# Kernel tuning notes

Hardware: AMD Instinct MI355X
Metric: run time of the kernel (lower is better)

## Reference

```python
import jax, jax.numpy as jnp
import numpy as np
from jax import lax

B, D, H, W = 1, 16, 128, 128
CIN, NPTS = 16, 100000
NEG = np.float32(-1e30)  # stands in for -inf at unoccupied voxels in max pooling


def _conv(x, wk):
    # Minkowski stride-1 conv at occupied sites == dense zero-padded conv masked to occupancy
    return lax.conv_general_dilated(x, wk, (1, 1, 1), 'SAME',
                                    dimension_numbers=('NCDHW', 'OIDHW', 'NCDHW'))


def _crelu(x, wk, occ):
    return jnp.where(occ, jax.nn.relu(_conv(x, wk)), 0.0)


def _mpool(x, occ, spatial):
    # Minkowski max pool: max over occupied voxels in the kernel window; output coords are
    # the stride-floored input coords (z halved). spatial=True -> kernel (3,3,3) else (3,1,1).
    xm = jnp.where(occ, x, NEG)
    win = (1, 1, 3, 3, 3) if spatial else (1, 1, 3, 1, 1)
    pad = [(0, 0), (0, 0), (1, 1), (1, 1), (1, 1)] if spatial else [(0, 0), (0, 0), (1, 1), (0, 0), (0, 0)]
    y = lax.reduce_window(xm, NEG, lax.max, win, (1, 1, 2, 1, 1), pad)
    occ2 = occ[:, :, 0::2] | occ[:, :, 1::2]
    return jnp.where(occ2, y, 0.0), occ2


def _forward(voxel_features, coors, ws, batch_size):
    b, d, h, w = coors[:, 0], coors[:, 1], coors[:, 2], coors[:, 3]
    cin = voxel_features.shape[1]
    grid = jnp.zeros((batch_size, D, H, W, cin), voxel_features.dtype).at[b, d, h, w].set(voxel_features)
    x = jnp.transpose(grid, (0, 4, 1, 2, 3))  # (B, C, D, H, W)
    occ = jnp.zeros((batch_size, 1, D, H, W), bool).at[b, 0, d, h, w].set(True)

    x = _crelu(x, ws[0], occ)
    x = _crelu(x, ws[1], occ)
    x, occ = _mpool(x, occ, True)
    for wk in ws[2:5]:
        x = _crelu(x, wk, occ)
    x, occ = _mpool(x, occ, True)
    for wk in ws[5:8]:
        x = _crelu(x, wk, occ)
    x, occ = _mpool(x, occ, False)  # kernel (3,1,1)
    n, c, dd, hh, ww = x.shape  # (B, 64, 2, H, W)
    return x.reshape(n, c * dd, hh, ww)


def setup_inputs():
    key = jax.random.key(0)
    ks = jax.random.split(key, 9)
    rng = np.random.default_rng(0)
    lin = rng.permutation(D * H * W)[:NPTS].astype(np.int64)  # unique occupied voxels
    d = (lin // (H * W)).astype(np.int32)
    h = ((lin // W) % H).astype(np.int32)
    w = (lin % W).astype(np.int32)
    coors = jnp.asarray(np.stack([np.zeros(NPTS, np.int32), d, h, w], axis=1))
    vf = jax.random.normal(ks[0], (NPTS, CIN), jnp.float32)

    def cw(k, o, i):
        return jax.random.normal(k, (o, i, 3, 3, 3), jnp.float32) * np.float32(1.0 / np.sqrt(i * 27))

    chans = [(32, CIN), (64, 32)] + [(64, 64)] * 6
    ws = {f"w{j + 1}": cw(ks[j + 1], o, i) for j, (o, i) in enumerate(chans)}
    return dict(voxel_features=vf, coors=coors, batch_size=B, **ws)


def reference(voxel_features, coors, batch_size, w1, w2, w3, w4, w5, w6, w7, w8):
    return _forward(voxel_features, coors, (w1, w2, w3, w4, w5, w6, w7, w8), batch_size)
```

## Files before the change

### kernel.cpp

```cpp
#include <hip/hip_runtime.h>
#include <stdint.h>

#define DEV __device__ __forceinline__

typedef float f32x4 __attribute__((ext_vector_type(4)));
typedef short s16x8 __attribute__((ext_vector_type(8)));
typedef unsigned int u32x4 __attribute__((ext_vector_type(4)));
typedef unsigned int u32x2 __attribute__((ext_vector_type(2)));

static constexpr int HM = 128, WM = 128;
static constexpr int HP = 130, WP = 130;

DEV unsigned short f2bf(float f) {
  unsigned int u = __float_as_uint(f);
  return (unsigned short)((u + 0x7fffu + ((u >> 16) & 1u)) >> 16);
}
DEV float bf2f(unsigned short s) { return __uint_as_float(((unsigned int)s) << 16); }

DEV void gll16(const void* g, void* l) {
  __builtin_amdgcn_global_load_lds((const unsigned int*)g, (unsigned int*)l, 16, 0, 0);
}

__global__ __launch_bounds__(256)
void scatter_k(const float* __restrict__ vf, const int* __restrict__ co,
               unsigned short* __restrict__ x,
               unsigned char* __restrict__ o0, unsigned char* __restrict__ o1,
               unsigned char* __restrict__ o2, unsigned char* __restrict__ o3,
               int npts) {
  int i = blockIdx.x * 256 + threadIdx.x;
  if (i >= npts) return;
  int d = co[i * 4 + 1], h = co[i * 4 + 2], w = co[i * 4 + 3];
  unsigned short* dst = x + (size_t)(((d + 1) * HP + (h + 1)) * WP + (w + 1)) * 32;
#pragma unroll
  for (int c = 0; c < 16; ++c) dst[c] = f2bf(vf[i * 16 + c]);
  int hw = h * WM + w;
  o0[d * (HM * WM) + hw] = 1;
  o1[(d >> 1) * (HM * WM) + hw] = 1;
  o2[(d >> 2) * (HM * WM) + hw] = 1;
  o3[(d >> 3) * (HM * WM) + hw] = 1;
}

__global__ __launch_bounds__(256)
void wcvt_all_k(const float* s0, const float* s1, const float* s2, const float* s3,
                const float* s4, const float* s5, const float* s6, const float* s7,
                unsigned short* __restrict__ dst) {
  int t = blockIdx.x * 256 + threadIdx.x;
  const int CIs[8] = {16, 32, 64, 64, 64, 64, 64, 64};
  const int CId[8] = {32, 32, 64, 64, 64, 64, 64, 64};
  const int COa[8] = {32, 64, 64, 64, 64, 64, 64, 64};
  const float* srcs[8] = {s0, s1, s2, s3, s4, s5, s6, s7};
  int start = 0;
#pragma unroll
  for (int i = 0; i < 8; ++i) {
    int sz = 27 * COa[i] * CId[i];
    if (t >= start && t < start + sz) {
      int l = t - start;
      int ci = l % CId[i];
      int r = l / CId[i];
      int cco = r % COa[i];
      int tap = r / COa[i];
      float v = (ci < CIs[i]) ? srcs[i][(cco * CIs[i] + ci) * 27 + tap] : 0.0f;
      dst[t] = f2bf(v);
    }
    start += sz;
  }
}

template <int CI, int CO>
__global__ __launch_bounds__(512, 2)
void conv_k(const unsigned short* __restrict__ xin, unsigned short* __restrict__ xout,
            const unsigned short* __restrict__ wt, const unsigned char* __restrict__ occ,
            int D) {
  constexpr int SLOTS = CI / 8;
  constexpr int CIB = CI / 32;
  constexpr int NM = CO / 16;
  constexpr int XV = 260;
  constexpr int NCX = 2 * 128 * SLOTS;
  constexpr int KX = NCX / 512;
  constexpr int NCW = 3 * CO * SLOTS;
  constexpr int KW = (NCW + 511) / 512;
  constexpr int VM = KX + KW;
  static_assert(VM == 3 || VM == 4 || VM == 7, "vmcnt literal");
  __shared__ __align__(16) unsigned short xs[2 * XV * CI];
  __shared__ __align__(16) unsigned short wls[2 * 3 * CO * CI];

  int nb = gridDim.x;
  int bid = blockIdx.x;
  int blk = (bid & 7) * (nb >> 3) + (bid >> 3);
  int tid = threadIdx.x;
  int nint = D * 64;

  int d = blk >> 6, h0 = (blk & 63) * 2;
  int lane = tid & 63, wv = tid >> 6, ln = lane & 15, lg = lane >> 4;

  unsigned short* xb0 = xs;
  unsigned short* xb1 = xs + XV * CI;
  unsigned short* wb0 = wls;
  unsigned short* wb1 = wls + 3 * CO * CI;

  auto issueX = [&](int kd, int kh, unsigned short* xbuf) {
#pragma unroll
    for (int i = 0; i < KX; ++i) {
      int c = i * 512 + tid;
      int r2 = c / (128 * SLOTS);
      int rem = c - r2 * 128 * SLOTS;
      int vv = rem / SLOTS;
      int sl = rem - vv * SLOTS;
      int vl = r2 * 130 + vv + 1;
      int ss = sl ^ (vl & (SLOTS - 1));
      const unsigned short* g =
          xin + ((size_t)((d + kd) * HP + (h0 + kh + r2)) * WP + (vv + 1)) * CI + ss * 8;
      gll16(g, xbuf + (size_t)(c + SLOTS * (1 + 2 * r2)) * 8);
    }
  };
  auto issueW = [&](int kd, int kh, unsigned short* wbuf) {
#pragma unroll
    for (int i = 0; i < KW; ++i) {
      int c = i * 512 + tid;
      if (c >= NCW) c -= NCW;
      int u = c / SLOTS, sl = c - (c / SLOTS) * SLOTS;
      int kw = u / CO, cc = u - kw * CO;
      int ss = sl ^ (u & (SLOTS - 1));
      const unsigned short* g =
          wt + ((size_t)((kd * 3 + kh) * 3 + kw) * CO + cc) * CI + ss * 8;
      gll16(g, wbuf + (size_t)c * 8);
    }
  };

  {
    const int hv4[4] = {0, 129, 130, 259};
    for (int t = tid; t < 2 * 4 * SLOTS; t += 512) {
      int b = t / (4 * SLOTS);
      int r = (t / SLOTS) & 3;
      int sl = t % SLOTS;
      *(u32x4*)((b ? xb1 : xb0) + (size_t)(hv4[r] * SLOTS + sl) * 8) = (u32x4)0u;
    }
  }
  issueX(0, 0, xb0);
  issueW(0, 0, wb0);

  {
    constexpr int CH8 = CO / 8;
    int hv = 2 * HP * WP + D * (2 * WP + 2 * HM);
    int tot8 = hv * CH8;
    int per = (tot8 + nint - 1) / nint;
    int base = blk * per, lim = base + per;
    if (lim > tot8) lim = tot8;
    for (int c = base + tid; c < lim; c += 512) {
      int i = c / CH8, sub = c - (c / CH8) * CH8;
      int p, hh, ww;
      if (i < 2 * HP * WP) {
        p = (i >= HP * WP) ? (D + 1) : 0;
        int rem = i - ((i >= HP * WP) ? HP * WP : 0);
        hh = rem / WP; ww = rem - hh * WP;
      } else {
        constexpr int PH = 2 * WP + 2 * HM;
        int j2 = i - 2 * HP * WP;
        p = j2 / PH + 1;
        int r2 = j2 - (p - 1) * PH;
        if (r2 < 2 * WP) { hh = (r2 >= WP) ? (HP - 1) : 0; ww = r2 % WP; }
        else { int r3 = r2 - 2 * WP; hh = 1 + (r3 & 127); ww = (r3 < HM) ? 0 : (WP - 1); }
      }
      *(u32x4*)(xout + ((size_t)(p * HP + hh) * WP + ww) * CO + sub * 8) = (u32x4)0u;
    }
  }

  float on[2];
#pragma unroll
  for (int j = 0; j < 2; ++j) {
    int vox = wv * 32 + j * 16 + ln;
    on[j] = occ[(d * HM + (h0 + (vox >> 7))) * WM + (vox & 127)] ? 1.0f : 0.0f;
  }

  f32x4 acc[NM][2];
#pragma unroll
  for (int m = 0; m < NM; ++m)
#pragma unroll
    for (int j = 0; j < 2; ++j) acc[m][j] = (f32x4)0.0f;

  asm volatile("s_waitcnt lgkmcnt(0)" ::: "memory");

  unsigned short *xc = xb0, *xn = xb1, *wc = wb0, *wn = wb1;
  for (int s = 0; s < 9; ++s) {
    if (s < 8) {
      int t = s + 1, kd = t / 3, kh = t % 3;
      issueX(kd, kh, xn);
      issueW(kd, kh, wn);
    }
    __builtin_amdgcn_sched_barrier(0);
    if (s < 8) {
      if constexpr (VM == 7) asm volatile("s_waitcnt vmcnt(7)" ::: "memory");
      else if constexpr (VM == 4) asm volatile("s_waitcnt vmcnt(4)" ::: "memory");
      else asm volatile("s_waitcnt vmcnt(3)" ::: "memory");
    } else {
      asm volatile("s_waitcnt vmcnt(0)" ::: "memory");
    }
    __builtin_amdgcn_sched_barrier(0);
    __builtin_amdgcn_s_barrier();
    __builtin_amdgcn_sched_barrier(0);
    __builtin_amdgcn_s_setprio(1);
#pragma unroll
    for (int kw = 0; kw < 3; ++kw) {
#pragma unroll
      for (int cb = 0; cb < CIB; ++cb) {
        int slot = cb * 4 + lg;
        s16x8 a[NM], b[2];
#pragma unroll
        for (int m = 0; m < NM; ++m) {
          int u = kw * CO + m * 16 + ln;
          a[m] = *(const s16x8*)(wc + ((size_t)u * SLOTS + (slot ^ (u & (SLOTS - 1)))) * 8);
        }
#pragma unroll
        for (int j = 0; j < 2; ++j) {
          int vox = wv * 32 + j * 16 + ln;
          int v = (vox >> 7) * 130 + (vox & 127) + kw;
          b[j] = *(const s16x8*)(xc + ((size_t)v * SLOTS + (slot ^ (v & (SLOTS - 1)))) * 8);
        }
#pragma unroll
        for (int m = 0; m < NM; ++m)
#pragma unroll
          for (int j = 0; j < 2; ++j)
            acc[m][j] = __builtin_amdgcn_mfma_f32_16x16x32_bf16(a[m], b[j], acc[m][j], 0, 0, 0);
      }
    }
    __builtin_amdgcn_s_setprio(0);
    if (s < 8) {
      __builtin_amdgcn_s_barrier();
      unsigned short* t1 = xc; xc = xn; xn = t1;
      unsigned short* t2 = wc; wc = wn; wn = t2;
    }
  }

#pragma unroll
  for (int j = 0; j < 2; ++j) {
    int vox = wv * 32 + j * 16 + ln;
    int r = vox >> 7, w2 = vox & 127;
    unsigned short* dst = xout + ((size_t)((d + 1) * HP + (h0 + r + 1)) * WP + (w2 + 1)) * CO;
#pragma unroll
    for (int m = 0; m < NM; ++m) {
      unsigned short q0 = f2bf(fmaxf(acc[m][j][0], 0.0f) * on[j]);
      unsigned short q1 = f2bf(fmaxf(acc[m][j][1], 0.0f) * on[j]);
      unsigned short q2 = f2bf(fmaxf(acc[m][j][2], 0.0f) * on[j]);
      unsigned short q3 = f2bf(fmaxf(acc[m][j][3], 0.0f) * on[j]);
      u32x2 pv;
      pv.x = (unsigned int)q0 | ((unsigned int)q1 << 16);
      pv.y = (unsigned int)q2 | ((unsigned int)q3 << 16);
      *(u32x2*)&dst[m * 16 + lg * 4] = pv;
    }
  }
}

template <int C>
__global__ __launch_bounds__(256)
void pool_sp_k(const unsigned short* __restrict__ xin, unsigned short* __restrict__ xout,
               const unsigned char* __restrict__ oc, int Dout) {
  constexpr int CH = C / 8;
  __shared__ __align__(16) unsigned short vm[WP * C];
  int row = blockIdx.x;
  int bh = row % HP, bdo = row / HP;
  int outRow = (bdo * HP + bh) * WP * C;
  int tid = threadIdx.x;
  if (bdo == 0 || bdo == Dout + 1 || bh == 0 || bh == HP - 1) {
    for (int i = tid; i < WP * C; i += 256) xout[outRow + i] = 0;
    return;
  }
  int dp = bdo - 1, h = bh - 1;

  for (int idx = tid; idx < WP * CH; idx += 256) {
    int w = idx / CH, c8 = idx - w * CH;
    float mx[8];
#pragma unroll
    for (int q = 0; q < 8; ++q) mx[q] = 0.0f;
#pragma unroll
    for (int dd = 0; dd < 3; ++dd)
#pragma unroll
      for (int hh = 0; hh < 3; ++hh) {
        const unsigned short* p =
            xin + ((size_t)((2 * dp + dd) * HP + (h + hh)) * WP + w) * C + c8 * 8;
        u32x4 v = *(const u32x4*)p;
        const unsigned short* u = (const unsigned short*)&v;
#pragma unroll
        for (int q = 0; q < 8; ++q) mx[q] = fmaxf(mx[q], bf2f(u[q]));
      }
    unsigned short o[8];
#pragma unroll
    for (int q = 0; q < 8; ++q) o[q] = f2bf(mx[q]);
    *(u32x4*)&vm[w * C + c8 * 8] = *(const u32x4*)o;
  }
  __syncthreads();

  for (int idx = tid; idx < WM * CH; idx += 256) {
    int w = idx / CH, c8 = idx - w * CH;
    float mx[8];
#pragma unroll
    for (int q = 0; q < 8; ++q) mx[q] = 0.0f;
#pragma unroll
    for (int ww = 0; ww < 3; ++ww) {
      u32x4 v = *(const u32x4*)&vm[(w + ww) * C + c8 * 8];
      const unsigned short* u = (const unsigned short*)&v;
#pragma unroll
      for (int q = 0; q < 8; ++q) mx[q] = fmaxf(mx[q], bf2f(u[q]));
    }
    bool on = oc[(dp * HM + h) * WM + w] != 0;
    unsigned short o[8];
#pragma unroll
    for (int q = 0; q < 8; ++q) o[q] = on ? f2bf(mx[q]) : (unsigned short)0;
    *(u32x4*)(xout + outRow + (w + 1) * C + c8 * 8) = *(const u32x4*)o;
  }
  for (int i = tid; i < 2 * C; i += 256) {
    int s = i / C, c = i - (i / C) * C;
    xout[outRow + (s ? (WP - 1) * C : 0) + c] = 0;
  }
}

__global__ __launch_bounds__(256)
void pool_d_k(const unsigned short* __restrict__ xin, float* __restrict__ out,
              const unsigned char* __restrict__ oc) {
  int t = blockIdx.x * 256 + threadIdx.x;
  int c8 = t & 7, w = (t >> 3) & 127, h = (t >> 10) & 127, dp = (t >> 17) & 1;
  float mx[8];
#pragma unroll
  for (int q = 0; q < 8; ++q) mx[q] = 0.0f;
#pragma unroll
  for (int dd = 0; dd < 3; ++dd) {
    const unsigned short* p =
        xin + ((size_t)((2 * dp + dd) * HP + (h + 1)) * WP + (w + 1)) * 64 + c8 * 8;
    u32x4 v = *(const u32x4*)p;
    const unsigned short* u = (const unsigned short*)&v;
#pragma unroll
    for (int q = 0; q < 8; ++q) mx[q] = fmaxf(mx[q], bf2f(u[q]));
  }
  bool on = oc[(dp * HM + h) * WM + w] != 0;
#pragma unroll
  for (int q = 0; q < 8; ++q) {
    int c = c8 * 8 + q;
    out[((c * 2 + dp) * HM + h) * WM + w] = on ? mx[q] : 0.0f;
  }
}

extern "C" void kernel_launch(void* const* d_in, const int* in_sizes, int n_in,
                              void* d_out, int out_size, void* d_ws, size_t ws_size,
                              hipStream_t stream) {
  (void)n_in; (void)out_size; (void)ws_size;
  const float* vf = (const float*)d_in[0];
  const int* co = (const int*)d_in[1];
  int npts = in_sizes[1] / 4;

  char* ws = (char*)d_ws;
  const size_t SA = (size_t)18 * 130 * 130 * 64 * 2;
  const size_t SB = (size_t)10 * 130 * 130 * 64 * 2;
  unsigned short* P = (unsigned short*)ws;
  unsigned short* Q = (unsigned short*)(ws + SA);
  unsigned short* R = P;
  unsigned char* occ0 = (unsigned char*)(ws + SA + SB);
  unsigned char* occ1 = occ0 + 16 * HM * WM;
  unsigned char* occ2 = occ1 + 8 * HM * WM;
  unsigned char* occ3 = occ2 + 4 * HM * WM;
  unsigned short* wb[8];
  {
    unsigned short* p = (unsigned short*)(occ3 + 2 * HM * WM);
    const int wsz[8] = {27 * 32 * 32, 27 * 64 * 32, 27 * 64 * 64, 27 * 64 * 64,
                        27 * 64 * 64, 27 * 64 * 64, 27 * 64 * 64, 27 * 64 * 64};
    for (int i = 0; i < 8; ++i) { wb[i] = p; p += wsz[i]; }
  }

  hipMemsetAsync(R, 0, (size_t)18 * 130 * 130 * 32 * 2, stream);
  hipMemsetAsync(occ0, 0, (size_t)(16 + 8 + 4 + 2) * HM * WM, stream);

  scatter_k<<<(npts + 255) / 256, 256, 0, stream>>>(vf, co, R, occ0, occ1, occ2, occ3, npts);

  {
    int tot = 27 * (32 * 32 + 64 * 32 + 6 * 64 * 64);
    wcvt_all_k<<<tot / 256, 256, 0, stream>>>(
        (const float*)d_in[3], (const float*)d_in[4], (const float*)d_in[5],
        (const float*)d_in[6], (const float*)d_in[7], (const float*)d_in[8],
        (const float*)d_in[9], (const float*)d_in[10], wb[0]);
  }

  conv_k<32, 32><<<16 * 64, 512, 0, stream>>>(R, Q, wb[0], occ0, 16);
  conv_k<32, 64><<<16 * 64, 512, 0, stream>>>(Q, P, wb[1], occ0, 16);
  pool_sp_k<64><<<10 * HP, 256, 0, stream>>>(P, Q, occ1, 8);
  conv_k<64, 64><<<8 * 64, 512, 0, stream>>>(Q, P, wb[2], occ1, 8);
  conv_k<64, 64><<<8 * 64, 512, 0, stream>>>(P, Q, wb[3], occ1, 8);
  conv_k<64, 64><<<8 * 64, 512, 0, stream>>>(Q, P, wb[4], occ1, 8);
  pool_sp_k<64><<<6 * HP, 256, 0, stream>>>(P, Q, occ2, 4);
  conv_k<64, 64><<<4 * 64, 512, 0, stream>>>(Q, P, wb[5], occ2, 4);
  conv_k<64, 64><<<4 * 64, 512, 0, stream>>>(P, Q, wb[6], occ2, 4);
  conv_k<64, 64><<<4 * 64, 512, 0, stream>>>(Q, P, wb[7], occ2, 4);
  pool_d_k<<<(2 * 128 * 128 * 8) / 256, 256, 0, stream>>>(P, (float*)d_out, occ3);
}
```

Measured before the change: 319.8 us.

## Reuse input rows across kh taps with ROWS-tall sliding LDS window

The conv kernel now holds ROWS+2 input rows per depth slice in LDS and reuses them across the three kh taps, loading only new rows per kd step instead of reloading two rows for every (kd,kh). Tile height is parameterized (4 rows for early layers, 2 for the last), with per-stage vmcnt waits matched to the new issue schedule. This cuts redundant global-to-LDS traffic but drops double buffering of the input tile and increases accumulator registers for ROWS=4, risking lower occupancy and exposed load latency.

```diff
diff --git a/kernel.cpp b/kernel.cpp
--- a/kernel.cpp
+++ b/kernel.cpp
@@ -19,6 +19,16 @@
 
 DEV void gll16(const void* g, void* l) {
   __builtin_amdgcn_global_load_lds((const unsigned int*)g, (unsigned int*)l, 16, 0, 0);
+}
+DEV void waitvmc(int n) {
+  if (n == 0)      asm volatile("s_waitcnt vmcnt(0)" ::: "memory");
+  else if (n == 1) asm volatile("s_waitcnt vmcnt(1)" ::: "memory");
+  else if (n == 2) asm volatile("s_waitcnt vmcnt(2)" ::: "memory");
+  else if (n == 3) asm volatile("s_waitcnt vmcnt(3)" ::: "memory");
+  else if (n == 4) asm volatile("s_waitcnt vmcnt(4)" ::: "memory");
+  else if (n == 5) asm volatile("s_waitcnt vmcnt(5)" ::: "memory");
+  else if (n == 7) asm volatile("s_waitcnt vmcnt(7)" ::: "memory");
+  else             asm volatile("s_waitcnt vmcnt(0)" ::: "memory");
 }
 
 __global__ __launch_bounds__(256)
@@ -66,51 +76,46 @@
   }
 }
 
-template <int CI, int CO>
-__global__ __launch_bounds__(512, 2)
+template <int CI, int CO, int ROWS>
+__global__ __launch_bounds__(512, 4)
 void conv_k(const unsigned short* __restrict__ xin, unsigned short* __restrict__ xout,
             const unsigned short* __restrict__ wt, const unsigned char* __restrict__ occ,
             int D) {
   constexpr int SLOTS = CI / 8;
+  constexpr int MSK = SLOTS - 1;
   constexpr int CIB = CI / 32;
   constexpr int NM = CO / 16;
-  constexpr int XV = 260;
-  constexpr int NCX = 2 * 128 * SLOTS;
-  constexpr int KX = NCX / 512;
+  constexpr int J = ROWS;
+  constexpr int XROWS = ROWS + 2;
+  constexpr int RXI = (128 * SLOTS) / 512;
   constexpr int NCW = 3 * CO * SLOTS;
   constexpr int KW = (NCW + 511) / 512;
-  constexpr int VM = KX + KW;
-  static_assert(VM == 3 || VM == 4 || VM == 7, "vmcnt literal");
-  __shared__ __align__(16) unsigned short xs[2 * XV * CI];
-  __shared__ __align__(16) unsigned short wls[2 * 3 * CO * CI];
+  constexpr int NA = 2 * RXI + KW;
+  constexpr int NB = RXI + KW;
+  constexpr int WOFF = 3 * CO * CI;
+  __shared__ __align__(16) unsigned short xs[XROWS * 130 * CI];
+  __shared__ __align__(16) unsigned short wls[2 * WOFF];
 
   int nb = gridDim.x;
   int bid = blockIdx.x;
   int blk = (bid & 7) * (nb >> 3) + (bid >> 3);
   int tid = threadIdx.x;
-  int nint = D * 64;
-
-  int d = blk >> 6, h0 = (blk & 63) * 2;
+  constexpr int HBLK = 128 / ROWS;
+  int d = blk / HBLK, hb = blk - (blk / HBLK) * HBLK;
+  int h0 = hb * ROWS;
   int lane = tid & 63, wv = tid >> 6, ln = lane & 15, lg = lane >> 4;
 
-  unsigned short* xb0 = xs;
-  unsigned short* xb1 = xs + XV * CI;
-  unsigned short* wb0 = wls;
-  unsigned short* wb1 = wls + 3 * CO * CI;
-
-  auto issueX = [&](int kd, int kh, unsigned short* xbuf) {
-#pragma unroll
-    for (int i = 0; i < KX; ++i) {
+  auto issueX = [&](int kd, int ri) {
+#pragma unroll
+    for (int i = 0; i < RXI; ++i) {
       int c = i * 512 + tid;
-      int r2 = c / (128 * SLOTS);
-      int rem = c - r2 * 128 * SLOTS;
-      int vv = rem / SLOTS;
-      int sl = rem - vv * SLOTS;
-      int vl = r2 * 130 + vv + 1;
-      int ss = sl ^ (vl & (SLOTS - 1));
+      int vcol = 1 + c / SLOTS;
+      int sl = c - (c / SLOTS) * SLOTS;
+      int v = ri * 130 + vcol;
+      int ss = sl ^ (v & MSK);
       const unsigned short* g =
-          xin + ((size_t)((d + kd) * HP + (h0 + kh + r2)) * WP + (vv + 1)) * CI + ss * 8;
-      gll16(g, xbuf + (size_t)(c + SLOTS * (1 + 2 * r2)) * 8);
+          xin + ((size_t)((d + kd) * HP + (h0 + ri)) * WP + vcol) * CI + ss * 8;
+      gll16(g, xs + (size_t)(ri * 130 + 1) * CI + (size_t)c * 8);
     }
   };
   auto issueW = [&](int kd, int kh, unsigned short* wbuf) {
@@ -120,30 +125,18 @@
       if (c >= NCW) c -= NCW;
       int u = c / SLOTS, sl = c - (c / SLOTS) * SLOTS;
       int kw = u / CO, cc = u - kw * CO;
-      int ss = sl ^ (u & (SLOTS - 1));
+      int ss = sl ^ (u & MSK);
       const unsigned short* g =
           wt + ((size_t)((kd * 3 + kh) * 3 + kw) * CO + cc) * CI + ss * 8;
       gll16(g, wbuf + (size_t)c * 8);
     }
   };
-
-  {
-    const int hv4[4] = {0, 129, 130, 259};
-    for (int t = tid; t < 2 * 4 * SLOTS; t += 512) {
-      int b = t / (4 * SLOTS);
-      int r = (t / SLOTS) & 3;
-      int sl = t % SLOTS;
-      *(u32x4*)((b ? xb1 : xb0) + (size_t)(hv4[r] * SLOTS + sl) * 8) = (u32x4)0u;
-    }
-  }
-  issueX(0, 0, xb0);
-  issueW(0, 0, wb0);
 
   {
     constexpr int CH8 = CO / 8;
     int hv = 2 * HP * WP + D * (2 * WP + 2 * HM);
     int tot8 = hv * CH8;
-    int per = (tot8 + nint - 1) / nint;
+    int per = (tot8 + nb - 1) / nb;
     int base = blk * per, lim = base + per;
     if (lim > tot8) lim = tot8;
     for (int c = base + tid; c < lim; c += 512) {
@@ -164,76 +157,88 @@
       *(u32x4*)(xout + ((size_t)(p * HP + hh) * WP + ww) * CO + sub * 8) = (u32x4)0u;
     }
   }
-
-  float on[2];
-#pragma unroll
-  for (int j = 0; j < 2; ++j) {
-    int vox = wv * 32 + j * 16 + ln;
+  issueX(0, 0);
+  issueX(0, 1);
+  issueW(0, 0, wls);
+  for (int t = tid; t < XROWS * 2 * SLOTS; t += 512) {
+    int ri = t / (2 * SLOTS);
+    int r2 = t - ri * 2 * SLOTS;
+    int colv = (r2 >= SLOTS) ? 129 : 0;
+    int sl = r2 & MSK;
+    *(u32x4*)(xs + (size_t)(ri * 130 + colv) * CI + sl * 8) = (u32x4)0u;
+  }
+  float on[J];
+#pragma unroll
+  for (int j = 0; j < J; ++j) {
+    int vox = wv * (16 * J) + j * 16 + ln;
     on[j] = occ[(d * HM + (h0 + (vox >> 7))) * WM + (vox & 127)] ? 1.0f : 0.0f;
   }
-
-  f32x4 acc[NM][2];
+  asm volatile("s_waitcnt lgkmcnt(0)" ::: "memory");
+
+  f32x4 acc[NM][J];
 #pragma unroll
   for (int m = 0; m < NM; ++m)
 #pragma unroll
-    for (int j = 0; j < 2; ++j) acc[m][j] = (f32x4)0.0f;
-
-  asm volatile("s_waitcnt lgkmcnt(0)" ::: "memory");
-
-  unsigned short *xc = xb0, *xn = xb1, *wc = wb0, *wn = wb1;
+    for (int j = 0; j < J; ++j) acc[m][j] = (f32x4)0.0f;
+
+#pragma unroll
   for (int s = 0; s < 9; ++s) {
-    if (s < 8) {
-      int t = s + 1, kd = t / 3, kh = t % 3;
-      issueX(kd, kh, xn);
-      issueW(kd, kh, wn);
+    int kd = s / 3, kh = s - 3 * kd;
+    unsigned short* wnext = wls + ((s + 1) & 1) * WOFF;
+    if (kh == 0) {
+#pragma unroll
+      for (int ri = 2; ri < XROWS; ++ri) issueX(kd, ri);
+      issueW(kd, 1, wnext);
+    } else if (kh == 1) {
+      if (kd < 2) issueX(kd + 1, 0);
+      issueW(kd, 2, wnext);
+    } else {
+      if (kd < 2) {
+        issueX(kd + 1, 1);
+        issueW(kd + 1, 0, wnext);
+      }
     }
     __builtin_amdgcn_sched_barrier(0);
-    if (s < 8) {
-      if constexpr (VM == 7) asm volatile("s_waitcnt vmcnt(7)" ::: "memory");
-      else if constexpr (VM == 4) asm volatile("s_waitcnt vmcnt(4)" ::: "memory");
-      else asm volatile("s_waitcnt vmcnt(3)" ::: "memory");
-    } else {
-      asm volatile("s_waitcnt vmcnt(0)" ::: "memory");
-    }
+    if (kh == 0)      waitvmc(NA);
+    else if (kh == 1) waitvmc(kd < 2 ? NB : KW);
+    else              waitvmc(kd < 2 ? NB : 0);
     __builtin_amdgcn_sched_barrier(0);
     __builtin_amdgcn_s_barrier();
     __builtin_amdgcn_sched_barrier(0);
+    const unsigned short* wc = wls + (s & 1) * WOFF;
     __builtin_amdgcn_s_setprio(1);
 #pragma unroll
     for (int kw = 0; kw < 3; ++kw) {
 #pragma unroll
       for (int cb = 0; cb < CIB; ++cb) {
         int slot = cb * 4 + lg;
-        s16x8 a[NM], b[2];
+        s16x8 a[NM], b[J];
 #pragma unroll
         for (int m = 0; m < NM; ++m) {
           int u = kw * CO + m * 16 + ln;
-          a[m] = *(const s16x8*)(wc + ((size_t)u * SLOTS + (slot ^ (u & (SLOTS - 1)))) * 8);
+          a[m] = *(const s16x8*)(wc + ((size_t)u * SLOTS + (slot ^ (u & MSK))) * 8);
         }
 #pragma unroll
-        for (int j = 0; j < 2; ++j) {
-          int vox = wv * 32 + j * 16 + ln;
-          int v = (vox >> 7) * 130 + (vox & 127) + kw;
-          b[j] = *(const s16x8*)(xc + ((size_t)v * SLOTS + (slot ^ (v & (SLOTS - 1)))) * 8);
+        for (int j = 0; j < J; ++j) {
+          int vox = wv * (16 * J) + j * 16 + ln;
+          int v = ((vox >> 7) + kh) * 130 + (vox & 127) + kw;
+          b[j] = *(const s16x8*)(xs + ((size_t)v * SLOTS + (slot ^ (v & MSK))) * 8);
         }
 #pragma unroll
         for (int m = 0; m < NM; ++m)
 #pragma unroll
-          for (int j = 0; j < 2; ++j)
+          for (int j = 0; j < J; ++j)
             acc[m][j] = __builtin_amdgcn_mfma_f32_16x16x32_bf16(a[m], b[j], acc[m][j], 0, 0, 0);
       }
     }
     __builtin_amdgcn_s_setprio(0);
-    if (s < 8) {
-      __builtin_amdgcn_s_barrier();
-      unsigned short* t1 = xc; xc = xn; xn = t1;
-      unsigned short* t2 = wc; wc = wn; wn = t2;
-    }
-  }
-
-#pragma unroll
-  for (int j = 0; j < 2; ++j) {
-    int vox = wv * 32 + j * 16 + ln;
+    __builtin_amdgcn_sched_barrier(0);
+    if (s < 8) __builtin_amdgcn_s_barrier();
+  }
+
+#pragma unroll
+  for (int j = 0; j < J; ++j) {
+    int vox = wv * (16 * J) + j * 16 + ln;
     int r = vox >> 7, w2 = vox & 127;
     unsigned short* dst = xout + ((size_t)((d + 1) * HP + (h0 + r + 1)) * WP + (w2 + 1)) * CO;
 #pragma unroll
@@ -377,15 +382,15 @@
         (const float*)d_in[9], (const float*)d_in[10], wb[0]);
   }
 
-  conv_k<32, 32><<<16 * 64, 512, 0, stream>>>(R, Q, wb[0], occ0, 16);
-  conv_k<32, 64><<<16 * 64, 512, 0, stream>>>(Q, P, wb[1], occ0, 16);
+  conv_k<32, 32, 4><<<16 * 32, 512, 0, stream>>>(R, Q, wb[0], occ0, 16);
+  conv_k<32, 64, 4><<<16 * 32, 512, 0, stream>>>(Q, P, wb[1], occ0, 16);
   pool_sp_k<64><<<10 * HP, 256, 0, stream>>>(P, Q, occ1, 8);
-  conv_k<64, 64><<<8 * 64, 512, 0, stream>>>(Q, P, wb[2], occ1, 8);
-  conv_k<64, 64><<<8 * 64, 512, 0, stream>>>(P, Q, wb[3], occ1, 8);
-  conv_k<64, 64><<<8 * 64, 512, 0, stream>>>(Q, P, wb[4], occ1, 8);
+  conv_k<64, 64, 4><<<8 * 32, 512, 0, stream>>>(Q, P, wb[2], occ1, 8);
+  conv_k<64, 64, 4><<<8 * 32, 512, 0, stream>>>(P, Q, wb[3], occ1, 8);
+  conv_k<64, 64, 4><<<8 * 32, 512, 0, stream>>>(Q, P, wb[4], occ1, 8);
   pool_sp_k<64><<<6 * HP, 256, 0, stream>>>(P, Q, occ2, 4);
-  conv_k<64, 64><<<4 * 64, 512, 0, stream>>>(Q, P, wb[5], occ2, 4);
-  conv_k<64, 64><<<4 * 64, 512, 0, stream>>>(P, Q, wb[6], occ2, 4);
-  conv_k<64, 64><<<4 * 64, 512, 0, stream>>>(Q, P, wb[7], occ2, 4);
+  conv_k<64, 64, 2><<<4 * 64, 512, 0, stream>>>(Q, P, wb[5], occ2, 4);
+  conv_k<64, 64, 2><<<4 * 64, 512, 0, stream>>>(P, Q, wb[6], occ2, 4);
+  conv_k<64, 64, 2><<<4 * 64, 512, 0, stream>>>(Q, P, wb[7], occ2, 4);
   pool_d_k<<<(2 * 128 * 128 * 8) / 256, 256, 0, stream>>>(P, (float*)d_out, occ3);
 }
```

After: 276.6 us (median of 2 runs). 1.16x faster.
